# Kernel tuning notes

Hardware: AMD Instinct MI355X
Metric: run time of the kernel (lower is better)

Reference implementation:

```python
import jax, jax.numpy as jnp
import numpy as np


def setup_inputs() -> dict:
    key = jax.random.key(0)
    ks = jax.random.split(key, 6)
    D, k, r = 4096, 16, 32  # embed_dim, low_rank_dimension, 2*low_rank_dimension
    B, S = 4, 4096
    return {
        "base": jax.random.normal(ks[0], (B, S, D), dtype=jnp.float32),
        "lora_A": jax.random.normal(ks[1], (k, D), dtype=jnp.float32),
        "lora_E": jax.random.normal(ks[2], (r, 1), dtype=jnp.float32),
        "lora_B": jax.random.normal(ks[3], (r, k), dtype=jnp.float32),
        "lora_aa": jax.random.normal(ks[4], (k, r), dtype=jnp.float32),
        "lora_bb": jax.random.normal(ks[5], (D, k), dtype=jnp.float32),
    }


def reference(base, lora_A, lora_E, lora_B, lora_aa, lora_bb):
    # Original math: base + base @ (A.T @ B.T @ diag(E) @ aa.T @ bb.T)
    #   result1 = A.T @ B.T  -> [D, r]
    #   result2 = aa.T @ bb.T -> [r, D]
    # Efficient equivalent: keep it low-rank; never build the [D, D] matrix
    # or the explicit diag. diag(E) @ result2 == E * result2 (row scaling).
    e = lora_E.reshape(-1)                              # [r]
    t = jnp.einsum('bsd,kd->bsk', base, lora_A)         # [B,S,k]  (base @ A.T)
    t = jnp.einsum('bsk,rk->bsr', t, lora_B)            # [B,S,r]  (.. @ B.T)
    t = t * e                                           # diag(E) scaling
    t = jnp.einsum('bsr,kr->bsk', t, lora_aa)           # [B,S,k]  (.. @ aa.T)
    delta = jnp.einsum('bsk,dk->bsd', t, lora_bb)       # [B,S,D]  (.. @ bb.T)
    return (base + delta).astype(base.dtype)
```

## Files before the change

### kernel.cpp

```cpp
#include <hip/hip_runtime.h>
#include <hip/hip_bf16.h>


#define D_DIM 4096
#define K_LR 16
#define R_LR 32
#define ROWS 64
#define NW 16
#define WWIN 256
#define DC 32
#define NCH (WWIN / DC)

typedef float f32x4 __attribute__((ext_vector_type(4)));

__global__ void __launch_bounds__(256) prep_kernel(const float* __restrict__ A,
                                                   const float* __restrict__ E,
                                                   const float* __restrict__ Bm,
                                                   const float* __restrict__ aa,
                                                   float* __restrict__ A2t) {
    __shared__ float Ms[K_LR][K_LR];
    const int t = threadIdx.x;
    {
        const int k = t >> 4, kp = t & 15;
        float s = 0.f;
        #pragma unroll
        for (int r = 0; r < R_LR; ++r)
            s += Bm[r * K_LR + k] * E[r] * aa[kp * R_LR + r];
        Ms[k][kp] = s;
    }
    __syncthreads();
    const int d = blockIdx.x * 256 + t;
    float acc[K_LR];
    #pragma unroll
    for (int kp = 0; kp < K_LR; ++kp) acc[kp] = 0.f;
    #pragma unroll
    for (int k = 0; k < K_LR; ++k) {
        const float a = A[k * D_DIM + d];
        #pragma unroll
        for (int kp = 0; kp < K_LR; ++kp) acc[kp] = fmaf(a, Ms[k][kp], acc[kp]);
    }
    #pragma unroll
    for (int kq = 0; kq < 4; ++kq) {
        f32x4 v = { acc[kq*4+0], acc[kq*4+1], acc[kq*4+2], acc[kq*4+3] };
        *(f32x4*)(A2t + (size_t)d * K_LR + kq * 4) = v;
    }
}

union ShA {
    float stage[NW][ROWS][DC];
    float tred[NW][ROWS][K_LR];
};

__global__ void __launch_bounds__(1024, 4) fused_kernel(const float* __restrict__ base,
                                                        const float* __restrict__ A2t,
                                                        const float* __restrict__ bb,
                                                        float* __restrict__ out, int N) {
    __shared__ ShA sh;
    __shared__ float tfin[ROWS][K_LR];
    const int tid  = threadIdx.x;
    const int lane = tid & 63;
    const int wv   = __builtin_amdgcn_readfirstlane(tid >> 6);
    const int r0   = blockIdx.x * ROWS;

    {
        const int a = lane >> 3;
        const int b = lane & 7;
        const int d0 = wv * WWIN;
        char* wbase = (char*)&sh.stage[wv][0][0];
        const int swz_w = 16 * (b ^ a);
        const int swz_r = (lane & 7) << 4;

        float acc[K_LR];
        #pragma unroll
        for (int k = 0; k < K_LR; ++k) acc[k] = 0.f;

        f32x4 st[8];
        #pragma unroll
        for (int i = 0; i < 8; ++i)
            st[i] = *(const f32x4*)(base + (size_t)(r0 + i*8 + a) * D_DIM + d0 + 4*b);

        for (int c = 0; c < NCH; ++c) {
            #pragma unroll
            for (int i = 0; i < 8; ++i)
                *(f32x4*)(wbase + (i*8 + a) * 128 + swz_w) = st[i];
            if (c + 1 < NCH) {
                const int dcn = d0 + (c + 1) * DC;
                #pragma unroll
                for (int i = 0; i < 8; ++i)
                    st[i] = *(const f32x4*)(base + (size_t)(r0 + i*8 + a) * D_DIM + dcn + 4*b);
            }
            const int dc = d0 + c * DC;
            #pragma unroll
            for (int j = 0; j < DC/4; ++j) {
                const f32x4 b4 = *(const f32x4*)(wbase + lane * 128 + ((16*j) ^ swz_r));
                const float* a2p = A2t + (size_t)(dc + 4*j) * K_LR;
                #pragma unroll
                for (int jj = 0; jj < 4; ++jj) {
                    const float bv = b4[jj];
                    #pragma unroll
                    for (int k = 0; k < K_LR; ++k)
                        acc[k] = fmaf(bv, a2p[jj * K_LR + k], acc[k]);
                }
            }
        }
        __syncthreads();
        #pragma unroll
        for (int kq = 0; kq < 4; ++kq) {
            f32x4 v = { acc[kq*4+0], acc[kq*4+1], acc[kq*4+2], acc[kq*4+3] };
            *(f32x4*)(&sh.tred[wv][lane][kq * 4]) = v;
        }
    }
    __syncthreads();
    {
        const int r = tid >> 4, k = tid & 15;
        float s = 0.f;
        #pragma unroll
        for (int w = 0; w < NW; ++w)
            s += sh.tred[w][r][k];
        tfin[r][k] = s;
    }
    __syncthreads();

    {
        const int cbase = tid * 4;
        const volatile f32x4* bbp = (const volatile f32x4*)(bb + (size_t)cbase * K_LR);
        f32x4 bbr[4][4];
        #pragma unroll
        for (int q = 0; q < 4; ++q)
            #pragma unroll
            for (int kq = 0; kq < 4; ++kq)
                bbr[q][kq] = bbp[q * 4 + kq];

        #pragma unroll 2
        for (int r = 0; r < ROWS; ++r) {
            f32x4 t16[4];
            #pragma unroll
            for (int kq = 0; kq < 4; ++kq)
                t16[kq] = *(const f32x4*)(&tfin[r][kq * 4]);

            const size_t row = (size_t)(r0 + r);
            const f32x4 bv = *(const f32x4*)(base + row * D_DIM + cbase);
            f32x4 ov;
            #pragma unroll
            for (int q = 0; q < 4; ++q) {
                float o = bv[q];
                #pragma unroll
                for (int k = 0; k < K_LR; ++k)
                    o = fmaf(t16[k >> 2][k & 3], bbr[q][k >> 2][k & 3], o);
                ov[q] = o;
            }
            __builtin_nontemporal_store(ov, (f32x4*)(out + row * D_DIM + cbase));
        }
    }
}

extern "C" void kernel_launch(void* const* d_in, const int* in_sizes, int n_in,
                              void* d_out, int out_size, void* d_ws, size_t ws_size,
                              hipStream_t stream) {
    const float* base = (const float*)d_in[0];
    const float* A    = (const float*)d_in[1];
    const float* E    = (const float*)d_in[2];
    const float* Bm   = (const float*)d_in[3];
    const float* aa   = (const float*)d_in[4];
    const float* bb   = (const float*)d_in[5];
    float* out = (float*)d_out;
    const int N = in_sizes[0] / D_DIM;

    float* A2t = (float*)d_ws;

    prep_kernel<<<D_DIM / 256, 256, 0, stream>>>(A, E, Bm, aa, A2t);
    fused_kernel<<<N / ROWS, 1024, 0, stream>>>(base, A2t, bb, out, N);
}
```

Measured before the change: 153.8 us.

## Restructure epilogue to reuse swizzled LDS staging with row-per-lane compute

The output phase used to keep per-thread bb columns in registers and loop over all 64 rows with strided per-row base reads. It now mirrors the first phase: each wave prefetches chunks of its column window into swizzled LDS, and each lane computes one row using its t vector in registers and wave-uniform bb loads. Results go back into the LDS slot, then out with coalesced nontemporal stores. The aim is better latency hiding on the second read of base through the software pipeline, at the cost of extra LDS traffic and register pressure.

Result: slower. 187.0 us (+21.6%).

```diff
diff --git a/kernel.cpp b/kernel.cpp
--- a/kernel.cpp
+++ b/kernel.cpp
@@ -62,14 +62,14 @@
     const int wv   = __builtin_amdgcn_readfirstlane(tid >> 6);
     const int r0   = blockIdx.x * ROWS;
 
+    const int a = lane >> 3;
+    const int b = lane & 7;
+    const int d0 = wv * WWIN;
+    char* wbase = (char*)&sh.stage[wv][0][0];
+    const int swz_w = 16 * (b ^ a);
+    const int swz_r = (lane & 7) << 4;
+
     {
-        const int a = lane >> 3;
-        const int b = lane & 7;
-        const int d0 = wv * WWIN;
-        char* wbase = (char*)&sh.stage[wv][0][0];
-        const int swz_w = 16 * (b ^ a);
-        const int swz_r = (lane & 7) << 4;
-
         float acc[K_LR];
         #pragma unroll
         for (int k = 0; k < K_LR; ++k) acc[k] = 0.f;
@@ -122,34 +122,52 @@
     __syncthreads();
 
     {
-        const int cbase = tid * 4;
-        const volatile f32x4* bbp = (const volatile f32x4*)(bb + (size_t)cbase * K_LR);
-        f32x4 bbr[4][4];
+        float t16[K_LR];
         #pragma unroll
-        for (int q = 0; q < 4; ++q)
+        for (int kq = 0; kq < 4; ++kq) {
+            const f32x4 v = *(const f32x4*)(&tfin[lane][kq * 4]);
+            t16[kq*4+0] = v[0]; t16[kq*4+1] = v[1];
+            t16[kq*4+2] = v[2]; t16[kq*4+3] = v[3];
+        }
+
+        f32x4 st[8];
+        #pragma unroll
+        for (int i = 0; i < 8; ++i)
+            st[i] = *(const f32x4*)(base + (size_t)(r0 + i*8 + a) * D_DIM + d0 + 4*b);
+
+        for (int c = 0; c < NCH; ++c) {
             #pragma unroll
-            for (int kq = 0; kq < 4; ++kq)
-                bbr[q][kq] = bbp[q * 4 + kq];
-
-        #pragma unroll 2
-        for (int r = 0; r < ROWS; ++r) {
-            f32x4 t16[4];
+            for (int i = 0; i < 8; ++i)
+                *(f32x4*)(wbase + (i*8 + a) * 128 + swz_w) = st[i];
+            if (c + 1 < NCH) {
+                const int dcn = d0 + (c + 1) * DC;
+                #pragma unroll
+                for (int i = 0; i < 8; ++i)
+                    st[i] = *(const f32x4*)(base + (size_t)(r0 + i*8 + a) * D_DIM + dcn + 4*b);
+            }
+            const int dc = d0 + c * DC;
             #pragma unroll
-            for (int kq = 0; kq < 4; ++kq)
-                t16[kq] = *(const f32x4*)(&tfin[r][kq * 4]);
-
-            const size_t row = (size_t)(r0 + r);
-            const f32x4 bv = *(const f32x4*)(base + row * D_DIM + cbase);
-            f32x4 ov;
+            for (int j = 0; j < DC/4; ++j) {
+                char* slot = wbase + lane * 128 + ((16*j) ^ swz_r);
+                const f32x4 b4 = *(const f32x4*)slot;
+                const float* bbs = bb + (size_t)(dc + 4*j) * K_LR;
+                f32x4 ov;
+                #pragma unroll
+                for (int q = 0; q < 4; ++q) {
+                    float o = b4[q];
+                    #pragma unroll
+                    for (int k = 0; k < K_LR; ++k)
+                        o = fmaf(t16[k], bbs[q * K_LR + k], o);
+                    ov[q] = o;
+                }
+                *(f32x4*)slot = ov;
+            }
             #pragma unroll
-            for (int q = 0; q < 4; ++q) {
-                float o = bv[q];
-                #pragma unroll
-                for (int k = 0; k < K_LR; ++k)
-                    o = fmaf(t16[k >> 2][k & 3], bbr[q][k >> 2][k & 3], o);
-                ov[q] = o;
+            for (int i = 0; i < 8; ++i) {
+                const f32x4 v = *(const f32x4*)(wbase + (i*8 + a) * 128 + swz_w);
+                __builtin_nontemporal_store(v,
+                    (f32x4*)(out + (size_t)(r0 + i*8 + a) * D_DIM + dc + 4*b));
             }
-            __builtin_nontemporal_store(ov, (f32x4*)(out + row * D_DIM + cbase));
         }
     }
 }
```
